# Optimization experiments

Hardware: AMD Instinct MI355X
Metric: run time of the kernel (lower is better)

## Reference

```python
import jax, jax.numpy as jnp
import numpy as np
from jax import lax

B, N, D = 4, 64, 32  # graphs, nodes/graph, volume side
HC = 1024            # hidden_channels
NF = 2048            # num_node_features = 32*(D//8)**3
NC = 4               # num_classes
LC = 256             # linear_channels = N*(HC//4)//64


def setup_inputs() -> dict:
    key = jax.random.key(0)
    ks = jax.random.split(key, 16)
    x = jax.random.normal(ks[0], (B, N, D, D, D), jnp.float32)
    # binary symmetric adjacency, zero diagonal (edge presence only; GCNConv ignores values)
    u = jax.random.uniform(ks[1], (B, N, N))
    a = (u < 0.2).astype(jnp.int32)
    a = jnp.maximum(a, a.transpose(0, 2, 1)) * (1 - jnp.eye(N, dtype=jnp.int32))
    s = 0.05
    inp = dict(
        x=x, adj=a, batch_size=B,
        w_conv1=jax.random.normal(ks[2], (16, 1, 3, 3, 3), jnp.float32) * s,
        b_conv1=jnp.zeros((16,), jnp.float32),
        w_conv2=jax.random.normal(ks[3], (32, 16, 3, 3, 3), jnp.float32) * s,
        b_conv2=jnp.zeros((32,), jnp.float32),
        w_g1=jax.random.normal(ks[4], (NF, HC), jnp.float32) * s,
        b_g1=jnp.zeros((HC,), jnp.float32),
        w_g2=jax.random.normal(ks[5], (HC, HC // 2), jnp.float32) * s,
        b_g2=jnp.zeros((HC // 2,), jnp.float32),
        w_g3=jax.random.normal(ks[6], (HC // 2, HC // 4), jnp.float32) * s,
        b_g3=jnp.zeros((HC // 4,), jnp.float32),
        w_fc1=jax.random.normal(ks[7], (LC, 2 * LC), jnp.float32) * s,
        b_fc1=jnp.zeros((2 * LC,), jnp.float32),
        w_fc2=jax.random.normal(ks[8], (2 * LC, NC), jnp.float32) * s,
        b_fc2=jnp.zeros((NC,), jnp.float32),
    )
    return inp


DN = ('NCDHW', 'OIDHW', 'NCDHW')


def _maxpool3(h):
    # MaxPool3d(kernel=3, stride=2, padding=1); pad value -inf matches torch
    return lax.reduce_window(h, -jnp.inf, lax.max,
                             (1, 1, 3, 3, 3), (1, 1, 2, 2, 2),
                             [(0, 0), (0, 0), (1, 1), (1, 1), (1, 1)])


def _gcn_norm(adj, dtype):
    # GCNConv: A_hat = A + I, sym-normalized D^-1/2 A_hat D^-1/2 (per graph)
    A = (adj != 0).astype(dtype) + jnp.eye(adj.shape[-1], dtype=dtype)[None]
    deg = A.sum(-1)                        # [B, N], >= 1
    dinv = deg ** -0.5
    return A * dinv[:, :, None] * dinv[:, None, :]


def _forward(x, adj, batch_size, w_conv1, b_conv1, w_conv2, b_conv2,
             w_g1, b_g1, w_g2, b_g2, w_g3, b_g3, w_fc1, b_fc1, w_fc2, b_fc2):
    b, n = x.shape[0], x.shape[1]
    v = x.reshape(b * n, 1, x.shape[2], x.shape[3], x.shape[4])
    h = lax.conv_general_dilated(v, w_conv1, (1, 1, 1), [(1, 1)] * 3, dimension_numbers=DN)
    h = jax.nn.relu(h + b_conv1[None, :, None, None, None])
    h = _maxpool3(h)                                     # [BN,16,16,16,16]
    h = lax.conv_general_dilated(h, w_conv2, (2, 2, 2), [(1, 1)] * 3, dimension_numbers=DN)
    h = jax.nn.relu(h + b_conv2[None, :, None, None, None])
    h = _maxpool3(h)                                     # [BN,32,4,4,4]
    feat = h.reshape(b, n, -1)                           # [B,N,2048]

    A_norm = _gcn_norm(adj, feat.dtype)                  # [B,N,N]
    gcn = lambda X, W, bb: jnp.einsum('bij,bjf->bif', A_norm, X @ W) + bb
    g = jax.nn.relu(gcn(feat, w_g1, b_g1))
    g = jax.nn.relu(gcn(g, w_g2, b_g2))
    g = gcn(g, w_g3, b_g3)                               # [B,N,256] (no relu, matches source)

    g = g.reshape(batch_size, -1)                        # [B, 16384]
    g = g.reshape(batch_size, -1, 64).max(-1)            # MaxPool1d(64) on 2D input -> [B,256]
    g = jax.nn.relu(g @ w_fc1 + b_fc1)
    return jax.nn.softmax(g @ w_fc2 + b_fc2, axis=-1)


def reference(x, adj, batch_size, w_conv1, b_conv1, w_conv2, b_conv2,
              w_g1, b_g1, w_g2, b_g2, w_g3, b_g3, w_fc1, b_fc1, w_fc2, b_fc2):
    return _forward(x, adj, batch_size, w_conv1, b_conv1, w_conv2, b_conv2,
                    w_g1, b_g1, w_g2, b_g2, w_g3, b_g3, w_fc1, b_fc1, w_fc2, b_fc2)
```

## Files before the change

### kernel.cpp

```cpp
#include <hip/hip_runtime.h>

typedef unsigned short ushort_t;
typedef unsigned long long ull_t;
typedef __attribute__((ext_vector_type(8))) short bf16x8;
typedef __attribute__((ext_vector_type(4))) float f32x4;

static __device__ __forceinline__ unsigned short f2bf(float f) {
  unsigned u = __float_as_uint(f);
  u = (u + 0x7FFFu + ((u >> 16) & 1u)) >> 16;
  return (unsigned short)u;
}

static __device__ __forceinline__ f32x4 max4(f32x4 a, f32x4 b) {
  f32x4 r;
  r[0] = fmaxf(a[0], b[0]); r[1] = fmaxf(a[1], b[1]);
  r[2] = fmaxf(a[2], b[2]); r[3] = fmaxf(a[3], b[3]);
  return r;
}

static __device__ __forceinline__ void gbar(int* bar0, int bid, int nb,
                                            bool do_wait) {
  __syncthreads();
  if (threadIdx.x == 0) {
    int* bar = bar0 + (bid << 10);
    __threadfence();
    const int leaf = (blockIdx.x & 7) << 5;
    const int nleaf = nb >> 3;
    if (__hip_atomic_fetch_add(&bar[leaf], 1, __ATOMIC_ACQ_REL,
                               __HIP_MEMORY_SCOPE_AGENT) == nleaf - 1) {
      if (__hip_atomic_fetch_add(&bar[256], 1, __ATOMIC_ACQ_REL,
                                 __HIP_MEMORY_SCOPE_AGENT) == 7) {
#pragma unroll
        for (int i = 0; i < 8; ++i)
          __hip_atomic_store(&bar[288 + (i << 5)], 1, __ATOMIC_RELEASE,
                             __HIP_MEMORY_SCOPE_AGENT);
      }
    }
    if (do_wait) {
      int* mygen = &bar[288 + leaf];
      for (int it = 0; it < (1 << 22); ++it) {
        if (__hip_atomic_load(mygen, __ATOMIC_RELAXED,
                              __HIP_MEMORY_SCOPE_AGENT) != 0) break;
        __builtin_amdgcn_s_sleep(2);
      }
      __threadfence();
    }
  }
  __syncthreads();
}


__device__ __forceinline__ void prep_transpose(
    const float* __restrict__ W, ushort_t* __restrict__ out,
    int K, int N, int n0, int k0, int t, float (*tile)[33])
{
  const int tx = t & 31, ty = t >> 5;
#pragma unroll
  for (int i = 0; i < 4; ++i) {
    const int k = k0 + ty + i * 8;
    tile[ty + i * 8][tx] = W[(size_t)k * N + n0 + tx];
  }
  __syncthreads();
#pragma unroll
  for (int i = 0; i < 4; ++i) {
    const int n = n0 + ty + i * 8;
    out[(size_t)n * K + k0 + tx] = f2bf(tile[tx][ty + i * 8]);
  }
}

__global__ __launch_bounds__(256) void k_prep(
    const float* __restrict__ x, ushort_t* __restrict__ xb16,
    const float* __restrict__ w2, ushort_t* __restrict__ w2f,
    const float* __restrict__ wg1, ushort_t* __restrict__ wg1T,
    const float* __restrict__ wg2, ushort_t* __restrict__ wg2T,
    const float* __restrict__ wg3, ushort_t* __restrict__ wg3T,
    const int* __restrict__ adj, float* __restrict__ An)
{
  __shared__ float tile[32][33];
  __shared__ float dinv[64];
  __shared__ int part[256];
  int b = blockIdx.x;
  const int t = threadIdx.x;
  if (b < 8192) {
    const int tid = b * 256 + t;
    const float4 v = ((const float4*)x)[tid];
    const unsigned lo = (unsigned)f2bf(v.x) | ((unsigned)f2bf(v.y) << 16);
    const unsigned hi = (unsigned)f2bf(v.z) | ((unsigned)f2bf(v.w) << 16);
    ((uint2*)xb16)[tid] = make_uint2(lo, hi);
    return;
  }
  b -= 8192;
  if (b < 56) {
    const int tid = b * 256 + t;
    if (tid < 14336) {
      const int nt = tid / 7168, rem = tid % 7168;
      const int kk = rem / 512, rem2 = rem % 512;
      const int l = rem2 >> 3, j = rem2 & 7;
      const int n = nt * 16 + (l & 15);
      const int k = (l >> 4) * 8 + kk * 32 + j;
      float v = 0.f;
      if (k < 432) v = w2[n * 432 + k];
      w2f[tid] = f2bf(v);
    }
    return;
  }
  b -= 56;
  if (b < 2048) { prep_transpose(wg1, wg1T, 2048, 1024, (b & 31) << 5, (b >> 5) << 5, t, tile); return; }
  b -= 2048;
  if (b < 512)  { prep_transpose(wg2, wg2T, 1024, 512,  (b & 15) << 5, (b >> 4) << 5, t, tile); return; }
  b -= 512;
  if (b < 128)  { prep_transpose(wg3, wg3T, 512,  256,  (b & 7)  << 5, (b >> 3) << 5, t, tile); return; }
  b -= 128;
  {
    const int i = t >> 2, q = t & 3;
    const int* ab = adj + b * 4096 + i * 64 + q * 16;
    int d = 0;
#pragma unroll
    for (int j = 0; j < 16; ++j) d += (ab[j] != 0) ? 1 : 0;
    part[t] = d;
    __syncthreads();
    if (q == 0)
      dinv[i] = rsqrtf((float)(1 + part[t] + part[t + 1] + part[t + 2] + part[t + 3]));
    __syncthreads();
    for (int idx = t; idx < 4096; idx += 256) {
      const int ii = idx >> 6, jj = idx & 63;
      const float a = (ii == jj) ? 1.f : ((adj[b * 4096 + idx] != 0) ? 1.f : 0.f);
      An[b * 4096 + idx] = a * dinv[ii] * dinv[jj];
    }
  }
}

__global__ __launch_bounds__(256) void k_conv1_mfma(
    const ushort_t* __restrict__ xb16, const float* __restrict__ wc,
    const float* __restrict__ bc, ushort_t* __restrict__ h1)
{
  __shared__ ushort_t L[2 * 34 * 76];
  char* Lb = (char*)L;
  const int bn = blockIdx.x >> 3, zg = blockIdx.x & 7;
  const int t = threadIdx.x;
  const int w = t >> 6, l = t & 63;
  const int grp = l >> 4, m = l & 15, ch = l & 15;
  const float NINF = -1e30f;

  union { short s[8]; bf16x8 v; } uA, uB;
#pragma unroll
  for (int j = 0; j < 8; ++j) {
    const int k = grp * 8 + j;
    float wA = 0.f, wB = 0.f;
    if (k < 12) {
      const int dx = k >> 2, dz = k & 3;
      if (dz < 3) { wA = wc[ch*27 + dz*9 + 0 + dx]; wB = wc[ch*27 + dz*9 + 6 + dx]; }
    } else if (k >= 16 && k < 28) {
      const int kk = k - 16, dx = kk >> 2, dz = kk & 3;
      if (dz < 3) wA = wc[ch*27 + dz*9 + 3 + dx];
    }
    uA.s[j] = (short)f2bf(wA);
    uB.s[j] = (short)f2bf(wB);
  }

  int aX1[3], aX2[3];
#pragma unroll
  for (int s = 0; s < 3; ++s) {
    const int Q1 = 2*m + s + 2*(grp & 1);
    const int Q2 = Q1 + 1;
    aX1[s] = (Q1 & 1) * 5168 + (Q1 >> 1) * 8;
    aX2[s] = (Q2 & 1) * 5168 + (Q2 >> 1) * 8;
  }
  const int rsel = (grp >> 1) * 152;

  for (int u = t; u < 200; u += 256) {
    int addr;
    if (u < 72) {
      const int rr = (u < 36) ? 0 : 33;
      const int s = (u < 36) ? u : u - 36;
      const int pp = s / 18, slot = s - pp * 18;
      addr = pp * 5168 + rr * 152 + slot * 8;
    } else {
      const int v = u - 72;
      const int rr = 1 + (v >> 2);
      const int pp = (v >> 1) & 1;
      const int slot = (v & 1) * 17;
      addr = pp * 5168 + rr * 152 + slot * 8;
    }
    *(ull_t*)(Lb + addr) = 0ull;
  }

  f32x4 accZ[4][2];
#pragma unroll
  for (int j = 0; j < 4; ++j)
#pragma unroll
    for (int p = 0; p < 2; ++p) accZ[j][p] = (f32x4){NINF, NINF, NINF, NINF};

  const ushort_t* xb = xb16 + (size_t)bn * 32768;

#pragma unroll 1
  for (int ci = 0; ci < 5; ++ci) {
    const int cz = 4*zg - 1 + ci;
    if (cz < 0) continue;
    if (t < 128) {
      const int r = 1 + (t >> 2), g = t & 3;
      const ushort_t* xrow = xb + (r - 1) * 32 + g * 8;
      uint4 u0 = make_uint4(0u, 0u, 0u, 0u), u2 = make_uint4(0u, 0u, 0u, 0u);
      if (cz > 0)  u0 = *(const uint4*)(xrow + (cz - 1) * 1024);
      const uint4 u1 = *(const uint4*)(xrow + cz * 1024);
      if (cz < 31) u2 = *(const uint4*)(xrow + (cz + 1) * 1024);
      char* b0 = Lb + r * 152 + (4 * g + 1) * 8;
      char* b1 = Lb + 5168 + r * 152 + (4 * g + 1) * 8;
      const unsigned* p0 = (const unsigned*)&u0;
      const unsigned* p1 = (const unsigned*)&u1;
      const unsigned* p2 = (const unsigned*)&u2;
#pragma unroll
      for (int e = 0; e < 4; ++e) {
        const unsigned w0 = p0[e], w1 = p1[e], w2v = p2[e];
        const unsigned lo_e = (w0 & 0xFFFFu) | (w1 << 16);
        const unsigned hi_e = (w2v & 0xFFFFu);
        const unsigned lo_o = (w0 >> 16) | (w1 & 0xFFFF0000u);
        const unsigned hi_o = (w2v >> 16);
        *(ull_t*)(b0 + e * 8) = (ull_t)lo_e | ((ull_t)hi_e << 32);
        *(ull_t*)(b1 + e * 8) = (ull_t)lo_o | ((ull_t)hi_o << 32);
      }
    }
    __syncthreads();
    f32x4 accP0 = (f32x4){NINF, NINF, NINF, NINF};
    f32x4 accP1 = (f32x4){NINF, NINF, NINF, NINF};
#pragma unroll
    for (int yy = 0; yy < 9; ++yy) {
      if (yy == 0 && w == 0) continue;
      const int y = 8 * w - 1 + yy;
      const int rbA = y * 152 + rsel;
      const int rbB = (y + 2) * 152;
      f32x4 Cy;
#pragma unroll
      for (int s = 0; s < 3; ++s) {
        union { ull_t u[2]; bf16x8 v; } fA, fB;
        fA.u[0] = *(const ull_t*)(Lb + aX1[s] + rbA);
        fA.u[1] = *(const ull_t*)(Lb + aX2[s] + rbA);
        fB.u[0] = *(const ull_t*)(Lb + aX1[s] + rbB);
        fB.u[1] = *(const ull_t*)(Lb + aX2[s] + rbB);
        f32x4 acc = (f32x4){0.f, 0.f, 0.f, 0.f};
        acc = __builtin_amdgcn_mfma_f32_16x16x32_bf16(fA.v, uA.v, acc, 0, 0, 0);
        acc = __builtin_amdgcn_mfma_f32_16x16x32_bf16(fB.v, uB.v, acc, 0, 0, 0);
        if (s == 0) acc[0] = (l < 16) ? NINF : acc[0];
        Cy = (s == 0) ? acc : max4(Cy, acc);
      }
      if (yy & 1) {
        const int c = (yy - 1) / 2;
        if ((c & 1) == 0) accP0 = max4(accP0, Cy); else accP1 = max4(accP1, Cy);
      } else {
        const int cl = yy / 2 - 1;
        const int chh = yy / 2;
        if (cl >= 0) {
          if ((cl & 1) == 0) {
            accP0 = max4(accP0, Cy);
            if (ci <= 2) accZ[cl][0] = max4(accZ[cl][0], accP0);
            if (ci >= 2) accZ[cl][1] = max4(accZ[cl][1], accP0);
            accP0 = (f32x4){NINF, NINF, NINF, NINF};
          } else {
            accP1 = max4(accP1, Cy);
            if (ci <= 2) accZ[cl][0] = max4(accZ[cl][0], accP1);
            if (ci >= 2) accZ[cl][1] = max4(accZ[cl][1], accP1);
            accP1 = (f32x4){NINF, NINF, NINF, NINF};
          }
        }
        if (chh <= 3) {
          if ((chh & 1) == 0) accP0 = max4(accP0, Cy); else accP1 = max4(accP1, Cy);
        }
      }
    }
    __syncthreads();
  }

  const float biasv = bc[ch];
#pragma unroll
  for (int j = 0; j < 4; ++j) {
    const int py = 4 * w + j;
#pragma unroll
    for (int p = 0; p < 2; ++p) {
      const int pz = 2 * zg + p;
      const f32x4 v = accZ[j][p];
      const unsigned lo = (unsigned)f2bf(fmaxf(v[0] + biasv, 0.f)) |
                          ((unsigned)f2bf(fmaxf(v[1] + biasv, 0.f)) << 16);
      const unsigned hi = (unsigned)f2bf(fmaxf(v[2] + biasv, 0.f)) |
                          ((unsigned)f2bf(fmaxf(v[3] + biasv, 0.f)) << 16);
      ushort_t* dst = h1 + (((size_t)(bn * 16 + ch) * 16 + pz) << 8) + py * 16 + grp * 4;
      *(uint2*)dst = make_uint2(lo, hi);
    }
  }
}

__global__ __launch_bounds__(128) void k_conv2(
    const ushort_t* __restrict__ h1, const ushort_t* __restrict__ w2f,
    ushort_t* __restrict__ c2b)
{
  __shared__ ushort_t U[16 * 456];
  ushort_t* Hs = U;
  unsigned* Hsd = (unsigned*)U;
  ushort_t* As = U;
  const int b = blockIdx.x;
  const int bn = b >> 5, oz = (b >> 2) & 7, yg = b & 3;
  const int t = threadIdx.x;
  const ushort_t* hb = h1 + ((size_t)bn << 16);
  const int w = t >> 6, l = t & 63;

  bf16x8 bfr[14];
#pragma unroll
  for (int kk = 0; kk < 14; ++kk)
    bfr[kk] = *(const bf16x8*)(const void*)&w2f[(((w * 14) + kk) * 64 + l) * 8];

#pragma unroll
  for (int it = 0; it < 9; ++it) {
    const int u = t + it * 128;
    const int row = u >> 2, q = u & 3;
    const int ic = row / 18;
    const int r2 = row - ic * 18;
    const int izp = r2 / 6;
    const int iyp = r2 - izp * 6;
    const int iz = 2 * oz - 1 + izp;
    const int iy = 4 * yg - 1 + iyp;
    uint2 v = make_uint2(0u, 0u);
    if ((unsigned)iz < 16u && (unsigned)iy < 16u)
      v = *(const uint2*)(hb + (ic << 12) + (iz << 8) + (iy << 4) + q * 4);
    *(uint2*)&Hs[row * 20 + q * 4] = v;
  }
  __syncthreads();

  const int m = t >> 3, sub = t & 7;
  const int ox = m & 7;
  const int my = (m >> 3) * 2;
  ushort_t tv[54];
  int j = 0;
#pragma unroll
  for (int ic2 = 0; ic2 < 2; ++ic2) {
    const int ic = sub * 2 + ic2;
#pragma unroll
    for (int dz = 0; dz < 3; ++dz) {
#pragma unroll
      for (int dy = 0; dy < 3; ++dy) {
        const int row = ic * 18 + dz * 6 + my + dy;
        const unsigned* rp = Hsd + row * 10;
        const unsigned d0 = (ox > 0) ? rp[ox - 1] : 0u;
        const unsigned d1 = rp[ox];
        tv[j]     = (ushort_t)(d0 >> 16);
        tv[j + 1] = (ushort_t)(d1 & 0xFFFFu);
        tv[j + 2] = (ushort_t)(d1 >> 16);
        j += 3;
      }
    }
  }
  __syncthreads();

  {
    unsigned* Aw = (unsigned*)As;
    const int wbase = m * 228 + sub * 27;
#pragma unroll
    for (int p = 0; p < 27; ++p)
      Aw[wbase + p] = (unsigned)tv[2 * p] | ((unsigned)tv[2 * p + 1] << 16);
    Aw[(t >> 3) * 228 + 216 + (t & 7)] = 0u;
  }
  __syncthreads();

  f32x4 acc = {0.f, 0.f, 0.f, 0.f};
  const ushort_t* arow = &As[(l & 15) * 456 + ((l >> 4) << 3)];
#pragma unroll
  for (int kk = 0; kk < 14; ++kk) {
    const bf16x8 af = *(const bf16x8*)(const void*)&arow[kk * 32];
    acc = __builtin_amdgcn_mfma_f32_16x16x32_bf16(af, bfr[kk], acc, 0, 0, 0);
  }
  const int n = w * 16 + (l & 15);
  const int m0 = (l >> 4) << 2;
  ushort_t* cb = c2b + (((size_t)(bn * 32 + n) * 8) + oz) * 64 + yg * 16 + m0;
  const unsigned lo = (unsigned)f2bf(acc[0]) | ((unsigned)f2bf(acc[1]) << 16);
  const unsigned hi = (unsigned)f2bf(acc[2]) | ((unsigned)f2bf(acc[3]) << 16);
  *(uint2*)cb = make_uint2(lo, hi);
}

__global__ __launch_bounds__(256) void k_pool2(
    const ushort_t* __restrict__ c2b, const float* __restrict__ bc2,
    ushort_t* __restrict__ featb, int* __restrict__ bar)
{
  if (blockIdx.x == 0) {
    for (int i = threadIdx.x; i < 4096; i += 256) bar[i] = 0;
  }
  const int tid = blockIdx.x * 256 + threadIdx.x;
  const int bn = tid >> 9, r = tid & 511;
  const int ch = r >> 4, pz = (r >> 2) & 3, py = r & 3;
  const ushort_t* base = c2b + ((size_t)(bn * 32 + ch) << 9);
  float m0 = -1e30f, m1 = -1e30f, m2 = -1e30f, m3 = -1e30f;
#pragma unroll
  for (int dz = 0; dz < 3; ++dz) {
    const int oz = 2 * pz - 1 + dz;
    if ((unsigned)oz >= 8u) continue;
#pragma unroll
    for (int dy = 0; dy < 3; ++dy) {
      const int oy = 2 * py - 1 + dy;
      if ((unsigned)oy >= 8u) continue;
      const uint4 v = *(const uint4*)(base + (oz << 6) + (oy << 3));
      const float x0 = __uint_as_float((v.x & 0xFFFFu) << 16);
      const float x1 = __uint_as_float(v.x & 0xFFFF0000u);
      const float x2 = __uint_as_float((v.y & 0xFFFFu) << 16);
      const float x3 = __uint_as_float(v.y & 0xFFFF0000u);
      const float x4 = __uint_as_float((v.z & 0xFFFFu) << 16);
      const float x5 = __uint_as_float(v.z & 0xFFFF0000u);
      const float x6 = __uint_as_float((v.w & 0xFFFFu) << 16);
      const float x7 = __uint_as_float(v.w & 0xFFFF0000u);
      m0 = fmaxf(m0, fmaxf(x0, x1));
      m1 = fmaxf(m1, fmaxf(x1, fmaxf(x2, x3)));
      m2 = fmaxf(m2, fmaxf(x3, fmaxf(x4, x5)));
      m3 = fmaxf(m3, fmaxf(x5, fmaxf(x6, x7)));
    }
  }
  const float bb = bc2[ch];
  const unsigned lo = (unsigned)f2bf(fmaxf(m0 + bb, 0.f)) |
                      ((unsigned)f2bf(fmaxf(m1 + bb, 0.f)) << 16);
  const unsigned hi = (unsigned)f2bf(fmaxf(m2 + bb, 0.f)) |
                      ((unsigned)f2bf(fmaxf(m3 + bb, 0.f)) << 16);
  *(uint2*)(featb + (size_t)bn * 2048 + r * 4) = make_uint2(lo, hi);
}

__device__ __forceinline__ void gcn_body(
    const ushort_t* __restrict__ Xb, const ushort_t* __restrict__ WT,
    const float* __restrict__ bias, const float* __restrict__ An,
    ushort_t* __restrict__ Ob, float* __restrict__ spw,
    int K, int N, int relu, int b, int jb,
    ushort_t (*As)[64 * 72], ushort_t (*Bs)[64 * 72], ushort_t* Ps)
{
  const int t = threadIdx.x, w = t >> 6, l = t & 63;
  const int r0 = t >> 3, kc0 = t & 7;
  const int lm = l & 15, lg = l >> 4;

  union { short s[8]; bf16x8 v; } afr[2];
  {
    const float* ap = An + b * 4096 + (16 * w + lm) * 64 + (lg << 3);
#pragma unroll
    for (int kc = 0; kc < 2; ++kc) {
      const float4 v0 = *(const float4*)(ap + kc * 32);
      const float4 v1 = *(const float4*)(ap + kc * 32 + 4);
      afr[kc].s[0] = (short)f2bf(v0.x); afr[kc].s[1] = (short)f2bf(v0.y);
      afr[kc].s[2] = (short)f2bf(v0.z); afr[kc].s[3] = (short)f2bf(v0.w);
      afr[kc].s[4] = (short)f2bf(v1.x); afr[kc].s[5] = (short)f2bf(v1.y);
      afr[kc].s[6] = (short)f2bf(v1.z); afr[kc].s[7] = (short)f2bf(v1.w);
    }
  }

  f32x4 acc[4];
#pragma unroll
  for (int nt = 0; nt < 4; ++nt) acc[nt] = (f32x4){0.f, 0.f, 0.f, 0.f};

  const ushort_t* arow0 = &Xb[(size_t)(b * 64 + r0) * K + kc0 * 8];
  const ushort_t* arow1 = &Xb[(size_t)(b * 64 + r0 + 32) * K + kc0 * 8];
  const ushort_t* brow0 = &WT[(size_t)(jb + r0) * K + kc0 * 8];
  const ushort_t* brow1 = &WT[(size_t)(jb + r0 + 32) * K + kc0 * 8];

  uint4 vaA0 = *(const uint4*)arow0;
  uint4 vaA1 = *(const uint4*)arow1;
  uint4 vbA0 = *(const uint4*)brow0;
  uint4 vbA1 = *(const uint4*)brow1;
  uint4 vaB0 = *(const uint4*)(arow0 + 64);
  uint4 vaB1 = *(const uint4*)(arow1 + 64);
  uint4 vbB0 = *(const uint4*)(brow0 + 64);
  uint4 vbB1 = *(const uint4*)(brow1 + 64);

  int buf = 0;
#pragma unroll 1
  for (int kt = 0; kt < K; kt += 128) {
    *(uint4*)&As[buf][r0 * 72 + kc0 * 8]        = vaA0;
    *(uint4*)&As[buf][(r0 + 32) * 72 + kc0 * 8] = vaA1;
    *(uint4*)&Bs[buf][r0 * 72 + kc0 * 8]        = vbA0;
    *(uint4*)&Bs[buf][(r0 + 32) * 72 + kc0 * 8] = vbA1;
    __syncthreads();
    if (kt + 128 < K) {
      vaA0 = *(const uint4*)(arow0 + kt + 128);
      vaA1 = *(const uint4*)(arow1 + kt + 128);
      vbA0 = *(const uint4*)(brow0 + kt + 128);
      vbA1 = *(const uint4*)(brow1 + kt + 128);
    }
#pragma unroll
    for (int ks = 0; ks < 2; ++ks) {
      const bf16x8 af = *(const bf16x8*)(const void*)
          &As[buf][(16 * w + lm) * 72 + ks * 32 + (lg << 3)];
#pragma unroll
      for (int nt = 0; nt < 4; ++nt) {
        const bf16x8 bf = *(const bf16x8*)(const void*)
            &Bs[buf][(nt * 16 + lm) * 72 + ks * 32 + (lg << 3)];
        acc[nt] = __builtin_amdgcn_mfma_f32_16x16x32_bf16(af, bf, acc[nt], 0, 0, 0);
      }
    }
    buf ^= 1;
    *(uint4*)&As[buf][r0 * 72 + kc0 * 8]        = vaB0;
    *(uint4*)&As[buf][(r0 + 32) * 72 + kc0 * 8] = vaB1;
    *(uint4*)&Bs[buf][r0 * 72 + kc0 * 8]        = vbB0;
    *(uint4*)&Bs[buf][(r0 + 32) * 72 + kc0 * 8] = vbB1;
    __syncthreads();
    if (kt + 192 < K) {
      vaB0 = *(const uint4*)(arow0 + kt + 192);
      vaB1 = *(const uint4*)(arow1 + kt + 192);
      vbB0 = *(const uint4*)(brow0 + kt + 192);
      vbB1 = *(const uint4*)(brow1 + kt + 192);
    }
#pragma unroll
    for (int ks = 0; ks < 2; ++ks) {
      const bf16x8 af = *(const bf16x8*)(const void*)
          &As[buf][(16 * w + lm) * 72 + ks * 32 + (lg << 3)];
#pragma unroll
      for (int nt = 0; nt < 4; ++nt) {
        const bf16x8 bf = *(const bf16x8*)(const void*)
            &Bs[buf][(nt * 16 + lm) * 72 + ks * 32 + (lg << 3)];
        acc[nt] = __builtin_amdgcn_mfma_f32_16x16x32_bf16(af, bf, acc[nt], 0, 0, 0);
      }
    }
    buf ^= 1;
  }

  __syncthreads();
  const int m0 = lg << 2;
#pragma unroll
  for (int nt = 0; nt < 4; ++nt) {
    const int n = nt * 16 + lm;
    const unsigned lo = (unsigned)f2bf(acc[nt][0]) | ((unsigned)f2bf(acc[nt][1]) << 16);
    const unsigned hi = (unsigned)f2bf(acc[nt][2]) | ((unsigned)f2bf(acc[nt][3]) << 16);
    *(uint2*)&Ps[n * 72 + 16 * w + m0] = make_uint2(lo, hi);
  }
  __syncthreads();

  float mx0 = -1e30f, mx1 = -1e30f, mx2 = -1e30f, mx3 = -1e30f;
#pragma unroll
  for (int nt = 0; nt < 4; ++nt) {
    const bf16x8 b0 = *(const bf16x8*)(const void*)&Ps[(nt * 16 + lm) * 72 + (lg << 3)];
    const bf16x8 b1 = *(const bf16x8*)(const void*)&Ps[(nt * 16 + lm) * 72 + 32 + (lg << 3)];
    f32x4 a2 = (f32x4){0.f, 0.f, 0.f, 0.f};
    a2 = __builtin_amdgcn_mfma_f32_16x16x32_bf16(afr[0].v, b0, a2, 0, 0, 0);
    a2 = __builtin_amdgcn_mfma_f32_16x16x32_bf16(afr[1].v, b1, a2, 0, 0, 0);
    const int col = jb + nt * 16 + lm;
    const float bv = bias[col];
    if (spw) {
      mx0 = fmaxf(mx0, a2[0] + bv);
      mx1 = fmaxf(mx1, a2[1] + bv);
      mx2 = fmaxf(mx2, a2[2] + bv);
      mx3 = fmaxf(mx3, a2[3] + bv);
    } else {
#pragma unroll
      for (int r = 0; r < 4; ++r) {
        const int row = b * 64 + 16 * w + m0 + r;
        float v = a2[r] + bv;
        if (relu) v = fmaxf(v, 0.f);
        Ob[(size_t)row * N + col] = f2bf(v);
      }
    }
  }
  if (spw) {
#pragma unroll
    for (int mk = 1; mk <= 8; mk <<= 1) {
      mx0 = fmaxf(mx0, __shfl_xor(mx0, mk));
      mx1 = fmaxf(mx1, __shfl_xor(mx1, mk));
      mx2 = fmaxf(mx2, __shfl_xor(mx2, mk));
      mx3 = fmaxf(mx3, __shfl_xor(mx3, mk));
    }
    if (lm == 0) {
      const int c = jb >> 6;
      const int n = 16 * w + m0;
      spw[b * 256 + (n + 0) * 4 + c] = mx0;
      spw[b * 256 + (n + 1) * 4 + c] = mx1;
      spw[b * 256 + (n + 2) * 4 + c] = mx2;
      spw[b * 256 + (n + 3) * 4 + c] = mx3;
    }
  }
}

__global__ __launch_bounds__(256) void k_tail(
    const ushort_t* __restrict__ featb,
    const ushort_t* __restrict__ wg1T, const float* __restrict__ bg1,
    const ushort_t* __restrict__ wg2T, const float* __restrict__ bg2,
    const ushort_t* __restrict__ wg3T, const float* __restrict__ bg3,
    const float* __restrict__ An,
    ushort_t* __restrict__ g1b, ushort_t* __restrict__ g2b,
    float* __restrict__ spw, float* __restrict__ shw,
    const float* __restrict__ w1, const float* __restrict__ b1,
    const float* __restrict__ w2, const float* __restrict__ b2,
    float* __restrict__ out, int* __restrict__ bar)
{
  __shared__ ushort_t As[2][64 * 72];
  __shared__ ushort_t Bs[2][64 * 72];
  __shared__ ushort_t Ps[64 * 72];
  __shared__ float red[260];
  const int bx = blockIdx.x, t = threadIdx.x;

  gcn_body(featb, wg1T, bg1, An, g1b, nullptr, 2048, 1024, 1,
           bx >> 4, (bx & 15) << 6, As, Bs, Ps);
  gbar(bar, 0, 64, bx < 32);

  if (bx < 32)
    gcn_body(g1b, wg2T, bg2, An, g2b, nullptr, 1024, 512, 1,
             bx >> 3, (bx & 7) << 6, As, Bs, Ps);
  gbar(bar, 1, 64, bx < 16);

  if (bx < 16)
    gcn_body(g2b, wg3T, bg3, An, nullptr, spw, 512, 256, 0,
             bx >> 2, (bx & 3) << 6, As, Bs, Ps);
  gbar(bar, 2, 64, true);

  {
    const int oo = t & 31, ks = t >> 5;
    const int bb = bx >> 4;
    const int jj = (bx & 15) * 32 + oo;
    const float* spb = spw + bb * 256;
    float s = 0.f;
#pragma unroll
    for (int i = 0; i < 32; ++i) {
      const int k = ks * 32 + i;
      s += spb[k] * w1[k * 512 + jj];
    }
    red[t] = s;
    __syncthreads();
    if (t < 32) {
      float s2 = 0.f;
#pragma unroll
      for (int i = 0; i < 8; ++i) s2 += red[t + i * 32];
      const int j2 = (bx & 15) * 32 + t;
      shw[bb * 512 + j2] = fmaxf(s2 + b1[j2], 0.f);
    }
  }
  gbar(bar, 3, 64, bx < 4);

  if (bx < 4) {
    float s = 0.f;
    if (t < 128) {
      const int c = t & 3, ks2 = t >> 2;
      const float* shb = shw + bx * 512;
#pragma unroll
      for (int i = 0; i < 16; ++i) {
        const int k = ks2 * 16 + i;
        s += shb[k] * w2[k * 4 + c];
      }
    }
    red[t] = s;
    __syncthreads();
    if (t < 4) {
      float s2 = b2[t];
#pragma unroll
      for (int i = 0; i < 32; ++i) s2 += red[t + i * 4];
      red[256 + t] = s2;
    }
    __syncthreads();
    if (t == 0) {
      const float a0 = red[256], a1 = red[257], a2v = red[258], a3 = red[259];
      const float mm = fmaxf(fmaxf(a0, a1), fmaxf(a2v, a3));
      const float e0 = expf(a0 - mm), e1 = expf(a1 - mm);
      const float e2 = expf(a2v - mm), e3 = expf(a3 - mm);
      const float inv = 1.f / (e0 + e1 + e2 + e3);
      out[bx * 4 + 0] = e0 * inv;
      out[bx * 4 + 1] = e1 * inv;
      out[bx * 4 + 2] = e2 * inv;
      out[bx * 4 + 3] = e3 * inv;
    }
  }
}

extern "C" void kernel_launch(void* const* d_in, const int* in_sizes, int n_in,
                              void* d_out, int out_size, void* d_ws, size_t ws_size,
                              hipStream_t stream)
{
  (void)in_sizes; (void)n_in; (void)out_size; (void)ws_size;
  const float* x   = (const float*)d_in[0];
  const int*   adj = (const int*)d_in[1];
  const float* wc1 = (const float*)d_in[3];
  const float* bc1 = (const float*)d_in[4];
  const float* wc2 = (const float*)d_in[5];
  const float* bc2 = (const float*)d_in[6];
  const float* wg1 = (const float*)d_in[7];
  const float* bg1 = (const float*)d_in[8];
  const float* wg2 = (const float*)d_in[9];
  const float* bg2 = (const float*)d_in[10];
  const float* wg3 = (const float*)d_in[11];
  const float* bg3 = (const float*)d_in[12];
  const float* wf1 = (const float*)d_in[13];
  const float* bf1 = (const float*)d_in[14];
  const float* wf2 = (const float*)d_in[15];
  const float* bf2 = (const float*)d_in[16];

  float* ws    = (float*)d_ws;
  ushort_t* h1 = (ushort_t*)d_ws;
  ushort_t* w2f   = (ushort_t*)(ws + 8388608);
  ushort_t* wg1Tb = (ushort_t*)(ws + 8395776);
  ushort_t* wg2Tb = (ushort_t*)(ws + 9444352);
  ushort_t* wg3Tb = (ushort_t*)(ws + 9706496);
  ushort_t* featb = (ushort_t*)(ws + 9772032);
  ushort_t* g1b   = (ushort_t*)(ws + 10034176);
  ushort_t* g2b   = (ushort_t*)(ws + 10165248);
  ushort_t* c2b  = (ushort_t*)(ws + 16777216);
  ushort_t* xb16 = (ushort_t*)(ws + 16777216);
  float* An   = ws + 21495808;
  float* spw  = ws + 2621440;
  float* shw  = ws + 2622464;
  int*   bar  = (int*)(ws + 22364160);
  float* outp = (float*)d_out;

  hipLaunchKernelGGL(k_prep,        dim3(10940),    dim3(256), 0, stream,
                     x, xb16, wc2, w2f, wg1, wg1Tb, wg2, wg2Tb, wg3, wg3Tb, adj, An);
  hipLaunchKernelGGL(k_conv1_mfma,  dim3(2048),     dim3(256), 0, stream, xb16, wc1, bc1, h1);
  hipLaunchKernelGGL(k_conv2,       dim3(8192),     dim3(128), 0, stream, h1, w2f, c2b);
  hipLaunchKernelGGL(k_pool2,       dim3(512),      dim3(256), 0, stream, c2b, bc2, featb, bar);
  hipLaunchKernelGGL(k_tail,        dim3(64),       dim3(256), 0, stream,
                     featb, wg1Tb, bg1, wg2Tb, bg2, wg3Tb, bg3, An, g1b, g2b,
                     spw, shw, wf1, bf1, wf2, bf2, outp, bar);
}
```

Before: 251.0 us.

## Fuse input bf16 conversion into conv1 and merge weight prep into one launch

The separate pass that converted the full input volume to bf16 is removed. conv1 now reads fp32 input directly and packs it to bf16 while staging into shared memory. The weight-transpose and adjacency-normalisation blocks are appended to the conv1 grid, so one launch replaces two. This removes a full write and re-read of the 32 MB input plus a launch boundary. In exchange conv1 reads twice the bytes per element (with halo reuse across z-slices), and the combined kernel carries extra LDS for the prep blocks.

```diff
diff --git a/kernel.cpp b/kernel.cpp
--- a/kernel.cpp
+++ b/kernel.cpp
@@ -9,6 +9,15 @@
   unsigned u = __float_as_uint(f);
   u = (u + 0x7FFFu + ((u >> 16) & 1u)) >> 16;
   return (unsigned short)u;
+}
+
+static __device__ __forceinline__ uint4 pack8(const float4 a, const float4 b) {
+  uint4 u;
+  u.x = (unsigned)f2bf(a.x) | ((unsigned)f2bf(a.y) << 16);
+  u.y = (unsigned)f2bf(a.z) | ((unsigned)f2bf(a.w) << 16);
+  u.z = (unsigned)f2bf(b.x) | ((unsigned)f2bf(b.y) << 16);
+  u.w = (unsigned)f2bf(b.z) | ((unsigned)f2bf(b.w) << 16);
+  return u;
 }
 
 static __device__ __forceinline__ f32x4 max4(f32x4 a, f32x4 b) {
@@ -68,76 +77,66 @@
   }
 }
 
-__global__ __launch_bounds__(256) void k_prep(
-    const float* __restrict__ x, ushort_t* __restrict__ xb16,
+__global__ __launch_bounds__(256) void k_pc1(
+    const float* __restrict__ x, const float* __restrict__ wc,
+    const float* __restrict__ bc, ushort_t* __restrict__ h1,
     const float* __restrict__ w2, ushort_t* __restrict__ w2f,
     const float* __restrict__ wg1, ushort_t* __restrict__ wg1T,
     const float* __restrict__ wg2, ushort_t* __restrict__ wg2T,
     const float* __restrict__ wg3, ushort_t* __restrict__ wg3T,
     const int* __restrict__ adj, float* __restrict__ An)
 {
+  __shared__ ushort_t L[2 * 34 * 76];
   __shared__ float tile[32][33];
   __shared__ float dinv[64];
   __shared__ int part[256];
-  int b = blockIdx.x;
   const int t = threadIdx.x;
-  if (b < 8192) {
-    const int tid = b * 256 + t;
-    const float4 v = ((const float4*)x)[tid];
-    const unsigned lo = (unsigned)f2bf(v.x) | ((unsigned)f2bf(v.y) << 16);
-    const unsigned hi = (unsigned)f2bf(v.z) | ((unsigned)f2bf(v.w) << 16);
-    ((uint2*)xb16)[tid] = make_uint2(lo, hi);
+
+  if (blockIdx.x >= 2048) {
+    int b = blockIdx.x - 2048;
+    if (b < 56) {
+      const int tid = b * 256 + t;
+      if (tid < 14336) {
+        const int nt = tid / 7168, rem = tid % 7168;
+        const int kk = rem / 512, rem2 = rem % 512;
+        const int l = rem2 >> 3, j = rem2 & 7;
+        const int n = nt * 16 + (l & 15);
+        const int k = (l >> 4) * 8 + kk * 32 + j;
+        float v = 0.f;
+        if (k < 432) v = w2[n * 432 + k];
+        w2f[tid] = f2bf(v);
+      }
+      return;
+    }
+    b -= 56;
+    if (b < 2048) { prep_transpose(wg1, wg1T, 2048, 1024, (b & 31) << 5, (b >> 5) << 5, t, tile); return; }
+    b -= 2048;
+    if (b < 512)  { prep_transpose(wg2, wg2T, 1024, 512,  (b & 15) << 5, (b >> 4) << 5, t, tile); return; }
+    b -= 512;
+    if (b < 128)  { prep_transpose(wg3, wg3T, 512,  256,  (b & 7)  << 5, (b >> 3) << 5, t, tile); return; }
+    b -= 128;
+    {
+      const int i = t >> 2, q = t & 3;
+      const int* ab = adj + b * 4096 + i * 64 + q * 16;
+      int d = 0;
+#pragma unroll
+      for (int j = 0; j < 16; ++j) d += (ab[j] != 0) ? 1 : 0;
+      part[t] = d;
+      __syncthreads();
+      if (q == 0)
+        dinv[i] = rsqrtf((float)(1 + part[t] + part[t + 1] + part[t + 2] + part[t + 3]));
+      __syncthreads();
+      for (int idx = t; idx < 4096; idx += 256) {
+        const int ii = idx >> 6, jj = idx & 63;
+        const float a = (ii == jj) ? 1.f : ((adj[b * 4096 + idx] != 0) ? 1.f : 0.f);
+        An[b * 4096 + idx] = a * dinv[ii] * dinv[jj];
+      }
+    }
     return;
   }
-  b -= 8192;
-  if (b < 56) {
-    const int tid = b * 256 + t;
-    if (tid < 14336) {
-      const int nt = tid / 7168, rem = tid % 7168;
-      const int kk = rem / 512, rem2 = rem % 512;
-      const int l = rem2 >> 3, j = rem2 & 7;
-      const int n = nt * 16 + (l & 15);
-      const int k = (l >> 4) * 8 + kk * 32 + j;
-      float v = 0.f;
-      if (k < 432) v = w2[n * 432 + k];
-      w2f[tid] = f2bf(v);
-    }
-    return;
-  }
-  b -= 56;
-  if (b < 2048) { prep_transpose(wg1, wg1T, 2048, 1024, (b & 31) << 5, (b >> 5) << 5, t, tile); return; }
-  b -= 2048;
-  if (b < 512)  { prep_transpose(wg2, wg2T, 1024, 512,  (b & 15) << 5, (b >> 4) << 5, t, tile); return; }
-  b -= 512;
-  if (b < 128)  { prep_transpose(wg3, wg3T, 512,  256,  (b & 7)  << 5, (b >> 3) << 5, t, tile); return; }
-  b -= 128;
-  {
-    const int i = t >> 2, q = t & 3;
-    const int* ab = adj + b * 4096 + i * 64 + q * 16;
-    int d = 0;
-#pragma unroll
-    for (int j = 0; j < 16; ++j) d += (ab[j] != 0) ? 1 : 0;
-    part[t] = d;
-    __syncthreads();
-    if (q == 0)
-      dinv[i] = rsqrtf((float)(1 + part[t] + part[t + 1] + part[t + 2] + part[t + 3]));
-    __syncthreads();
-    for (int idx = t; idx < 4096; idx += 256) {
-      const int ii = idx >> 6, jj = idx & 63;
-      const float a = (ii == jj) ? 1.f : ((adj[b * 4096 + idx] != 0) ? 1.f : 0.f);
-      An[b * 4096 + idx] = a * dinv[ii] * dinv[jj];
-    }
-  }
-}
-
-__global__ __launch_bounds__(256) void k_conv1_mfma(
-    const ushort_t* __restrict__ xb16, const float* __restrict__ wc,
-    const float* __restrict__ bc, ushort_t* __restrict__ h1)
-{
-  __shared__ ushort_t L[2 * 34 * 76];
+
   char* Lb = (char*)L;
   const int bn = blockIdx.x >> 3, zg = blockIdx.x & 7;
-  const int t = threadIdx.x;
   const int w = t >> 6, l = t & 63;
   const int grp = l >> 4, m = l & 15, ch = l & 15;
   const float NINF = -1e30f;
@@ -191,19 +190,30 @@
 #pragma unroll
     for (int p = 0; p < 2; ++p) accZ[j][p] = (f32x4){NINF, NINF, NINF, NINF};
 
-  const ushort_t* xb = xb16 + (size_t)bn * 32768;
-
 #pragma unroll 1
   for (int ci = 0; ci < 5; ++ci) {
     const int cz = 4*zg - 1 + ci;
     if (cz < 0) continue;
     if (t < 128) {
       const int r = 1 + (t >> 2), g = t & 3;
-      const ushort_t* xrow = xb + (r - 1) * 32 + g * 8;
+      const float* xrow = x + (size_t)bn * 32768 + (r - 1) * 32 + g * 8;
       uint4 u0 = make_uint4(0u, 0u, 0u, 0u), u2 = make_uint4(0u, 0u, 0u, 0u);
-      if (cz > 0)  u0 = *(const uint4*)(xrow + (cz - 1) * 1024);
-      const uint4 u1 = *(const uint4*)(xrow + cz * 1024);
-      if (cz < 31) u2 = *(const uint4*)(xrow + (cz + 1) * 1024);
+      uint4 u1;
+      if (cz > 0) {
+        const float4 a = *(const float4*)(xrow + (cz - 1) * 1024);
+        const float4 c = *(const float4*)(xrow + (cz - 1) * 1024 + 4);
+        u0 = pack8(a, c);
+      }
+      {
+        const float4 a = *(const float4*)(xrow + cz * 1024);
+        const float4 c = *(const float4*)(xrow + cz * 1024 + 4);
+        u1 = pack8(a, c);
+      }
+      if (cz < 31) {
+        const float4 a = *(const float4*)(xrow + (cz + 1) * 1024);
+        const float4 c = *(const float4*)(xrow + (cz + 1) * 1024 + 4);
+        u2 = pack8(a, c);
+      }
       char* b0 = Lb + r * 152 + (4 * g + 1) * 8;
       char* b1 = Lb + 5168 + r * 152 + (4 * g + 1) * 8;
       const unsigned* p0 = (const unsigned*)&u0;
@@ -687,19 +697,18 @@
   ushort_t* g1b   = (ushort_t*)(ws + 10034176);
   ushort_t* g2b   = (ushort_t*)(ws + 10165248);
   ushort_t* c2b  = (ushort_t*)(ws + 16777216);
-  ushort_t* xb16 = (ushort_t*)(ws + 16777216);
   float* An   = ws + 21495808;
   float* spw  = ws + 2621440;
   float* shw  = ws + 2622464;
   int*   bar  = (int*)(ws + 22364160);
   float* outp = (float*)d_out;
 
-  hipLaunchKernelGGL(k_prep,        dim3(10940),    dim3(256), 0, stream,
-                     x, xb16, wc2, w2f, wg1, wg1Tb, wg2, wg2Tb, wg3, wg3Tb, adj, An);
-  hipLaunchKernelGGL(k_conv1_mfma,  dim3(2048),     dim3(256), 0, stream, xb16, wc1, bc1, h1);
-  hipLaunchKernelGGL(k_conv2,       dim3(8192),     dim3(128), 0, stream, h1, w2f, c2b);
-  hipLaunchKernelGGL(k_pool2,       dim3(512),      dim3(256), 0, stream, c2b, bc2, featb, bar);
-  hipLaunchKernelGGL(k_tail,        dim3(64),       dim3(256), 0, stream,
+  hipLaunchKernelGGL(k_pc1,   dim3(4796), dim3(256), 0, stream,
+                     x, wc1, bc1, h1, wc2, w2f, wg1, wg1Tb, wg2, wg2Tb,
+                     wg3, wg3Tb, adj, An);
+  hipLaunchKernelGGL(k_conv2, dim3(8192), dim3(128), 0, stream, h1, w2f, c2b);
+  hipLaunchKernelGGL(k_pool2, dim3(512),  dim3(256), 0, stream, c2b, bc2, featb, bar);
+  hipLaunchKernelGGL(k_tail,  dim3(64),   dim3(256), 0, stream,
                      featb, wg1Tb, bg1, wg2Tb, bg2, wg3Tb, bg3, An, g1b, g2b,
                      spw, shw, wf1, bf1, wf2, bf2, outp, bar);
 }
```

Result: faster. 239.7 us (median of 2 runs) (-4.5%).
